# Kernel optimization log

Hardware: AMD Instinct MI355X
Metric: run time of the kernel (lower is better)

## Reference

```python
import jax, jax.numpy as jnp
import numpy as np

B, H, W, C_IN, C_OUT, KH, KW = 32, 56, 56, 128, 256, 3, 3


def setup_inputs() -> dict:
    key = jax.random.key(0)
    k1, k2, k3 = jax.random.split(key, 3)
    x = jax.random.normal(k1, (B, H, W, C_IN), dtype=jnp.float32)
    w = jax.random.normal(k2, (KH, KW, C_IN, C_OUT), dtype=jnp.float32) * 0.05
    b = jax.random.normal(k3, (C_OUT,), dtype=jnp.float32) * 0.05
    return {"x": x, "w": w, "b": b}


def reference(x, w, b):
    # SAME-padded, stride-1 2D conv (math identical to the im2col loop in the
    # original, collapsed into a single conv/GEMM) plus bias.
    out = jax.lax.conv_general_dilated(
        x, w,
        window_strides=(1, 1),
        padding="SAME",
        dimension_numbers=("NHWC", "HWIO", "NHWC"),
    )
    return out + b
```

## Files before the change

kernel.cpp:

```cpp
#include <hip/hip_runtime.h>

#define B_ 32
#define CI 128
#define CO 256
#define K_DIM 1152
#define M_DIM 100352
#define BM 128
#define BN 128
#define BK 32
#define KTILES 36
#define HPAD 58
#define XB_OFF 589824

typedef float          floatx4  __attribute__((ext_vector_type(4)));
typedef unsigned short ushortx8 __attribute__((ext_vector_type(8)));
typedef __bf16         bf16x8   __attribute__((ext_vector_type(8)));

typedef __attribute__((address_space(1))) void gas_void;
typedef __attribute__((address_space(3))) void las_void;
#define GLD16(g, l) __builtin_amdgcn_global_load_lds( \
    (gas_void*)(uintptr_t)(g), (las_void*)(l), 16, 0, 0)

__device__ __forceinline__ unsigned short bf16_rne(float f) {
    unsigned u = __builtin_bit_cast(unsigned, f);
    u += 0x7FFFu + ((u >> 16) & 1u);
    return (unsigned short)(u >> 16);
}

__global__ void wt_transpose_kernel(const float* __restrict__ w,
                                    unsigned short* __restrict__ wt) {
    __shared__ unsigned short tile[64][65];
    const int kt = blockIdx.x * 64, nt = blockIdx.y * 64;
    #pragma unroll
    for (int i = 0; i < 16; ++i) {
        int idx = i * 256 + threadIdx.x;
        int kl = idx >> 6, nl = idx & 63;
        tile[kl][nl] = bf16_rne(w[(size_t)(kt + kl) * CO + nt + nl]);
    }
    __syncthreads();
    #pragma unroll
    for (int i = 0; i < 16; ++i) {
        int idx = i * 256 + threadIdx.x;
        int nl = idx >> 6, kl = idx & 63;
        wt[(size_t)(nt + nl) * K_DIM + kt + kl] = tile[kl][nl];
    }
}

__global__ void xpad_kernel(const float* __restrict__ x,
                            unsigned short* __restrict__ xb) {
    const int t   = blockIdx.x * 256 + threadIdx.x;
    const int pix = t >> 4;
    const int cc  = (t & 15) << 3;
    const int b   = pix / (HPAD * HPAD);
    const int rem = pix % (HPAD * HPAD);
    const int hp  = rem / HPAD, wp = rem % HPAD;
    ushortx8 g = {0, 0, 0, 0, 0, 0, 0, 0};
    if (hp >= 1 && hp <= 56 && wp >= 1 && wp <= 56) {
        const float* s = x + ((size_t)((b * 56 + hp - 1) * 56 + (wp - 1))) * CI + cc;
        floatx4 f0 = ((const floatx4*)s)[0];
        floatx4 f1 = ((const floatx4*)s)[1];
        #pragma unroll
        for (int e = 0; e < 4; ++e) { g[e] = bf16_rne(f0[e]); g[e + 4] = bf16_rne(f1[e]); }
    }
    *(ushortx8*)(xb + (size_t)pix * CI + cc) = g;
}

__global__ __launch_bounds__(256, 2)
void conv_gemm_kernel(const unsigned short* __restrict__ xb,
                      const unsigned short* __restrict__ wt,
                      const float* __restrict__ bias,
                      float* __restrict__ out) {
    __shared__ unsigned short As[2][BM * BK];
    __shared__ unsigned short Bs[2][BN * BK];

    const int tid  = threadIdx.x;
    const int bx   = blockIdx.x;
    const int by   = blockIdx.y;
    const int wid  = tid >> 6;
    const int lane = tid & 63;
    const int lrow = lane & 15;
    const int quad = lane >> 4;
    const int wm   = (wid & 1) * 64;
    const int wn   = (wid >> 1) * 64;

    const int rseg = lane >> 2;
    const int cglb = ((lane & 3) - (rseg >> 1)) & 3;

    const int ar0 = wid * 32 + rseg;
    const int ar1 = ar0 + 16;
    const int m0 = by * BM + ar0;
    const int m1 = by * BM + ar1;
    const int b0 = m0 / 3136, r0 = m0 % 3136;
    const int b1 = m1 / 3136, r1 = m1 % 3136;
    const unsigned short* ag0 = xb + ((size_t)((b0 * HPAD + r0 / 56) * HPAD + r0 % 56)) * CI + cglb * 8;
    const unsigned short* ag1 = xb + ((size_t)((b1 * HPAD + r1 / 56) * HPAD + r1 % 56)) * CI + cglb * 8;
    const unsigned short* bg0 = wt + (size_t)(bx * BN + ar0) * K_DIM + cglb * 8;
    const unsigned short* bg1 = wt + (size_t)(bx * BN + ar1) * K_DIM + cglb * 8;

    const int ldsA0 = (wid * 32) * BK;
    const int ldsA1 = ldsA0 + 16 * BK;

    const int swz = ((quad + (lrow >> 1)) & 3) * 8;
    int a_idx[4], b_idx[4];
    #pragma unroll
    for (int i = 0; i < 4; ++i) {
        a_idx[i] = (wm + i * 16 + lrow) * BK + swz;
        b_idx[i] = (wn + i * 16 + lrow) * BK + swz;
    }

    floatx4 acc[4][4] = {};

    auto stage = [&](int kb, int buf) {
        const int p    = kb >> 2;
        const int c0   = (kb & 3) << 5;
        const int aoff = (p / 3 * HPAD + p % 3) * CI + c0;
        const int boff = kb * BK;
        GLD16(ag0 + aoff, &As[buf][ldsA0]);
        GLD16(ag1 + aoff, &As[buf][ldsA1]);
        GLD16(bg0 + boff, &Bs[buf][ldsA0]);
        GLD16(bg1 + boff, &Bs[buf][ldsA1]);
    };

    auto compute = [&](int buf) {
        ushortx8 arv[4], brv[4];
        #pragma unroll
        for (int mi = 0; mi < 4; ++mi) arv[mi] = *(const ushortx8*)&As[buf][a_idx[mi]];
        #pragma unroll
        for (int ni = 0; ni < 4; ++ni) brv[ni] = *(const ushortx8*)&Bs[buf][b_idx[ni]];
        #pragma unroll
        for (int mi = 0; mi < 4; ++mi)
            #pragma unroll
            for (int ni = 0; ni < 4; ++ni)
                acc[mi][ni] = __builtin_amdgcn_mfma_f32_16x16x32_bf16(
                    __builtin_bit_cast(bf16x8, arv[mi]),
                    __builtin_bit_cast(bf16x8, brv[ni]),
                    acc[mi][ni], 0, 0, 0);
    };

    stage(0, 0);
    __syncthreads();
    int cur = 0;
    #pragma unroll 1
    for (int kb = 0; kb < KTILES - 1; ++kb) {
        stage(kb + 1, cur ^ 1);
        compute(cur);
        __syncthreads();
        cur ^= 1;
    }
    compute(cur);

    float bv[4];
    #pragma unroll
    for (int ni = 0; ni < 4; ++ni)
        bv[ni] = bias[bx * BN + wn + ni * 16 + lrow];

    #pragma unroll
    for (int mi = 0; mi < 4; ++mi) {
        #pragma unroll
        for (int r = 0; r < 4; ++r) {
            const int row = by * BM + wm + mi * 16 + quad * 4 + r;
            float* o = out + (size_t)row * CO + bx * BN + wn + lrow;
            #pragma unroll
            for (int ni = 0; ni < 4; ++ni)
                o[ni * 16] = acc[mi][ni][r] + bv[ni];
        }
    }
}

extern "C" void kernel_launch(void* const* d_in, const int* in_sizes, int n_in,
                              void* d_out, int out_size, void* d_ws, size_t ws_size,
                              hipStream_t stream) {
    (void)in_sizes; (void)n_in; (void)out_size; (void)ws_size;
    const float* x    = (const float*)d_in[0];
    const float* w    = (const float*)d_in[1];
    const float* bias = (const float*)d_in[2];
    float* out = (float*)d_out;

    unsigned short* wt = (unsigned short*)d_ws;
    unsigned short* xb = (unsigned short*)((char*)d_ws + XB_OFF);

    wt_transpose_kernel<<<dim3(K_DIM / 64, CO / 64), dim3(256), 0, stream>>>(w, wt);
    xpad_kernel<<<dim3((B_ * HPAD * HPAD * 16) / 256), dim3(256), 0, stream>>>(x, xb);
    conv_gemm_kernel<<<dim3(2, M_DIM / BM), dim3(256), 0, stream>>>(xb, wt, bias, out);
}
```

Baseline: 215.1 us.

## Widen GEMM tile to cover all output channels with 512-thread blocks

BN goes from 128 to 256, so each block now computes every output channel for its 128 rows and the grid becomes 1D over M. The block doubles to 8 waves. Each wave now loads one A row-segment and two B row-segments, so the input tile is read from global memory once instead of once per N-tile. The launch bound is raised to (512, 6). That occupancy hint may squeeze the register budget for the 64 accumulator floats per thread and cause spills, while the 48KB of LDS per block already limits how many blocks fit on a CU.

```diff
diff --git a/kernel.cpp b/kernel.cpp
--- a/kernel.cpp
+++ b/kernel.cpp
@@ -6,7 +6,7 @@
 #define K_DIM 1152
 #define M_DIM 100352
 #define BM 128
-#define BN 128
+#define BN 256
 #define BK 32
 #define KTILES 36
 #define HPAD 58
@@ -65,7 +65,7 @@
     *(ushortx8*)(xb + (size_t)pix * CI + cc) = g;
 }
 
-__global__ __launch_bounds__(256, 2)
+__global__ __launch_bounds__(512, 6)
 void conv_gemm_kernel(const unsigned short* __restrict__ xb,
                       const unsigned short* __restrict__ wt,
                       const float* __restrict__ bias,
@@ -74,8 +74,7 @@
     __shared__ unsigned short Bs[2][BN * BK];
 
     const int tid  = threadIdx.x;
-    const int bx   = blockIdx.x;
-    const int by   = blockIdx.y;
+    const int by   = blockIdx.x;
     const int wid  = tid >> 6;
     const int lane = tid & 63;
     const int lrow = lane & 15;
@@ -86,19 +85,18 @@
     const int rseg = lane >> 2;
     const int cglb = ((lane & 3) - (rseg >> 1)) & 3;
 
-    const int ar0 = wid * 32 + rseg;
-    const int ar1 = ar0 + 16;
-    const int m0 = by * BM + ar0;
-    const int m1 = by * BM + ar1;
+    const int ar = wid * 16 + rseg;
+    const int m0 = by * BM + ar;
     const int b0 = m0 / 3136, r0 = m0 % 3136;
-    const int b1 = m1 / 3136, r1 = m1 % 3136;
     const unsigned short* ag0 = xb + ((size_t)((b0 * HPAD + r0 / 56) * HPAD + r0 % 56)) * CI + cglb * 8;
-    const unsigned short* ag1 = xb + ((size_t)((b1 * HPAD + r1 / 56) * HPAD + r1 % 56)) * CI + cglb * 8;
-    const unsigned short* bg0 = wt + (size_t)(bx * BN + ar0) * K_DIM + cglb * 8;
-    const unsigned short* bg1 = wt + (size_t)(bx * BN + ar1) * K_DIM + cglb * 8;
 
-    const int ldsA0 = (wid * 32) * BK;
-    const int ldsA1 = ldsA0 + 16 * BK;
+    const int nr0 = wid * 32 + rseg;
+    const unsigned short* bg0 = wt + (size_t)nr0 * K_DIM + cglb * 8;
+    const unsigned short* bg1 = bg0 + (size_t)16 * K_DIM;
+
+    const int ldsA  = (wid * 16) * BK;
+    const int ldsB0 = (wid * 32) * BK;
+    const int ldsB1 = ldsB0 + 16 * BK;
 
     const int swz = ((quad + (lrow >> 1)) & 3) * 8;
     int a_idx[4], b_idx[4];
@@ -115,10 +113,9 @@
         const int c0   = (kb & 3) << 5;
         const int aoff = (p / 3 * HPAD + p % 3) * CI + c0;
         const int boff = kb * BK;
-        GLD16(ag0 + aoff, &As[buf][ldsA0]);
-        GLD16(ag1 + aoff, &As[buf][ldsA1]);
-        GLD16(bg0 + boff, &Bs[buf][ldsA0]);
-        GLD16(bg1 + boff, &Bs[buf][ldsA1]);
+        GLD16(ag0 + aoff, &As[buf][ldsA]);
+        GLD16(bg0 + boff, &Bs[buf][ldsB0]);
+        GLD16(bg1 + boff, &Bs[buf][ldsB1]);
     };
 
     auto compute = [&](int buf) {
@@ -152,14 +149,14 @@
     float bv[4];
     #pragma unroll
     for (int ni = 0; ni < 4; ++ni)
-        bv[ni] = bias[bx * BN + wn + ni * 16 + lrow];
+        bv[ni] = bias[wn + ni * 16 + lrow];
 
     #pragma unroll
     for (int mi = 0; mi < 4; ++mi) {
         #pragma unroll
         for (int r = 0; r < 4; ++r) {
             const int row = by * BM + wm + mi * 16 + quad * 4 + r;
-            float* o = out + (size_t)row * CO + bx * BN + wn + lrow;
+            float* o = out + (size_t)row * CO + wn + lrow;
             #pragma unroll
             for (int ni = 0; ni < 4; ++ni)
                 o[ni * 16] = acc[mi][ni][r] + bv[ni];
@@ -181,5 +178,5 @@
 
     wt_transpose_kernel<<<dim3(K_DIM / 64, CO / 64), dim3(256), 0, stream>>>(w, wt);
     xpad_kernel<<<dim3((B_ * HPAD * HPAD * 16) / 256), dim3(256), 0, stream>>>(x, xb);
-    conv_gemm_kernel<<<dim3(2, M_DIM / BM), dim3(256), 0, stream>>>(xb, wt, bias, out);
+    conv_gemm_kernel<<<dim3(M_DIM / BM), dim3(512), 0, stream>>>(xb, wt, bias, out);
 }
```

Result: slower. 436.7 us (+103.0%).
